# Kernel tuning notes

Measured on AMD Instinct MI355X. Metric: run time of the kernel, lower is better.

Reference implementation:

```python
import jax, jax.numpy as jnp
import numpy as np

IMAGE_W = 256
IMAGE_H = 256
SIGMA = 0.2
EPS = 1e-07


def _gauss_filter(g, size, psize, pad):
    """g: [B,N] center coords in pixels. Returns [B,N,size,psize]."""
    # grid coords over padded canvas: value i - pad at row i (matches np.indices - pad)
    coords = jnp.arange(size + 2 * pad, dtype=jnp.float32) - pad          # [size+2pad]
    offs = jnp.arange(1, psize + 1, dtype=jnp.float32) - psize / 2 - 0.5  # [psize]
    mu = g[:, :, None] + offs[None, None, :]                              # [B,N,psize]
    F = jnp.exp(-(coords[None, None, :, None] - mu[:, :, None, :]) ** 2 / (2 * SIGMA ** 2))
    F = F / (F.sum(axis=2, keepdims=True) + EPS)
    return F[:, :, pad:size + pad]                                        # [B,N,size,psize]


def setup_inputs() -> dict:
    key = jax.random.key(0)
    k1, k2 = jax.random.split(key)
    brushes = jax.random.uniform(k1, (32, 64, 2), dtype=jnp.float32)
    patches = jax.random.normal(k2, (32, 64, 3, 16, 16), dtype=jnp.float32)
    return {"brushes": brushes, "patches": patches}


def reference(brushes, patches):
    B, N, C, ph, pw = patches.shape
    pad = ph // 2  # pad='half_patch'
    gx = brushes[:, :, 0] * IMAGE_W  # [B,N]
    gy = brushes[:, :, 1] * IMAGE_H
    Fx = _gauss_filter(gx, IMAGE_W, pw, pad)  # [B,N,w,pw]
    Fy = _gauss_filter(gy, IMAGE_H, ph, pad)  # [B,N,h,ph]
    # contract over pw: [B,N,C,w,ph]
    t = jnp.einsum('bnwq,bncpq->bncwp', Fx, patches)
    # contract over ph: [B,N,C,w,h]
    out = jnp.einsum('bncwp,bnhp->bncwh', t, Fy)
    out = out.mean(axis=1)            # [B,C,w,h]
    out = jnp.swapaxes(out, 2, 3)     # [B,C,h,w]
    return out
```

## Files before the change

### kernel.cpp

```cpp
#include <hip/hip_runtime.h>
#include <hip/hip_bf16.h>


#define E25 1.3887944e-11f

__global__ __launch_bounds__(256) void brush_prep(
        const float* __restrict__ brushes,
        const float* __restrict__ patches,
        float* __restrict__ patchP)
{
    const int bn   = blockIdx.x;
    const int tid  = threadIdx.x;
    const int lane = tid & 63;
    const int qi   = tid & 15;
    const int pi   = tid >> 4;

    const float2 g = ((const float2*)brushes)[bn];
    const float gx = g.x * 256.0f, gy = g.y * 256.0f;

    const int k = lane & 31;
    const float gg = (k >> 4) ? gy : gx;
    const float mu = gg + (float)(k & 15) - 7.5f;
    const float fl = floorf(mu);
    float Z = 0.0f;
#pragma unroll
    for (int d = -1; d <= 2; ++d) {
        const float c = fl + (float)d;
        if (c >= -8.0f && c <= 263.0f) {
            const float u = c - mu;
            Z += __expf(-12.5f * u * u);
        }
    }
    const float invz = 1.0f / (Z + 1e-7f);
    const float s = __shfl(invz, qi, 64) * __shfl(invz, 16 + pi, 64);

    const float* pb = patches + (size_t)bn * 768;
    float*       wp = patchP  + (size_t)bn * 768;
    wp[tid]       = pb[tid]       * s;
    wp[tid + 256] = pb[tid + 256] * s;
    wp[tid + 512] = pb[tid + 512] * s;
}

__global__ __launch_bounds__(256) void brush_tile(
        const float* __restrict__ brushes,
        const float* __restrict__ patchP,
        float* __restrict__ out)
{
    const int b    = blockIdx.z;
    const int tx   = blockIdx.x << 4;
    const int ty   = blockIdx.y << 4;
    const int tid  = threadIdx.x;
    const int lane = tid & 63;
    const int qi   = tid & 15;
    const int pi   = tid >> 4;
    const int w    = tx + qi;
    const int h    = ty + pi;

    __shared__ float4 T4[2 * 16 * 21];

    if (tid < 160) {
        const int buf = tid / 80, r = tid % 80;
        T4[buf * 336 + (r / 5) * 21 + 16 + (r % 5)] = make_float4(0, 0, 0, 0);
    }

    const float2 g0 = ((const float2*)brushes)[(b << 6) + lane];
    const float bx = g0.x * 256.0f, by = g0.y * 256.0f;
    const bool hit =
        (bx >= (float)tx - 9.5f) & (bx <= (float)tx + 24.5f) &
        (by >= (float)ty - 9.5f) & (by <= (float)ty + 24.5f);
    unsigned long long mask = __ballot(hit);

    float acc0 = 0.0f, acc1 = 0.0f, acc2 = 0.0f;

    if (mask) {
        int n = __builtin_ctzll(mask);
        mask &= mask - 1;
        const float* wp = patchP + (size_t)((b << 6) + n) * 768;
        float a0 = wp[tid], a1 = wp[tid + 256], a2 = wp[tid + 512];
        int it = 0;

        while (true) {
            int nn = -1;
            float p0, p1, p2;
            if (mask) {
                nn = __builtin_ctzll(mask);
                mask &= mask - 1;
                const float* wq = patchP + (size_t)((b << 6) + nn) * 768;
                p0 = wq[tid]; p1 = wq[tid + 256]; p2 = wq[tid + 512];
            }

            const float gx = __shfl(bx, n, 64);
            const float gy = __shfl(by, n, 64);
            const int buf = (it & 1) * 336;

            {
                const float ax  = (float)w - gx + 7.5f;
                const bool  okx = (ax >= -2.5f) & (ax <= 17.5f);
                int qlo = (int)ceilf(ax - 2.0f);
                qlo = qlo < 0 ? 0 : (qlo > 15 ? 15 : qlo);
                float d0 = ax - (float)qlo;
                d0 = fminf(fmaxf(d0, -3.0f), 3.0f);
                float wgt = okx ? __expf(-12.5f * d0 * d0) : 0.0f;
                float u   = __expf(25.0f * d0 - 12.5f);
                const int base = ((pi & 3) << 4) + qlo;
                float4 s = make_float4(0, 0, 0, 0);
#pragma unroll
                for (int j = 0; j < 5; ++j) {
                    const float t0 = __shfl(a0, base + j, 64);
                    const float t1 = __shfl(a1, base + j, 64);
                    const float t2 = __shfl(a2, base + j, 64);
                    const float wj = (qlo + j < 16) ? wgt : 0.0f;
                    s.x += wj * t0; s.y += wj * t1; s.z += wj * t2;
                    wgt *= u; u *= E25;
                }
                T4[buf + qi * 21 + pi] = s;
            }
            __syncthreads();

            {
                const float ay = (float)h - gy + 7.5f;
                if (ay >= -2.5f && ay <= 17.5f) {
                    int plo = (int)ceilf(ay - 2.0f);
                    plo = plo < 0 ? 0 : (plo > 15 ? 15 : plo);
                    const float d0 = ay - (float)plo;
                    float wgt = __expf(-12.5f * d0 * d0);
                    float u   = __expf(25.0f * d0 - 12.5f);
                    const float4* row = &T4[buf + qi * 21 + plo];
#pragma unroll
                    for (int j = 0; j < 5; ++j) {
                        const float4 v = row[j];
                        acc0 += wgt * v.x; acc1 += wgt * v.y; acc2 += wgt * v.z;
                        wgt *= u; u *= E25;
                    }
                }
            }

            if (nn < 0) break;
            n = nn; a0 = p0; a1 = p1; a2 = p2; ++it;
        }
    }

    const float sc = 1.0f / 64.0f;
    float* ob = out + (((size_t)(b * 3)) << 16) + (h << 8) + w;
    ob[0]       = acc0 * sc;
    ob[1 << 16] = acc1 * sc;
    ob[2 << 16] = acc2 * sc;
}

extern "C" void kernel_launch(void* const* d_in, const int* in_sizes, int n_in,
                              void* d_out, int out_size, void* d_ws, size_t ws_size,
                              hipStream_t stream) {
    const float* brushes = (const float*)d_in[0];
    const float* patches = (const float*)d_in[1];
    float* out    = (float*)d_out;
    float* patchP = (float*)d_ws;
    brush_prep<<<dim3(32 * 64), dim3(256), 0, stream>>>(brushes, patches, patchP);
    brush_tile<<<dim3(16, 16, 32), dim3(256), 0, stream>>>(brushes, patchP, out);
}
```

Before: 81.55 us.

## Fuse patch normalization into tile kernel and process 8-tile vertical strips per block

Removes the separate prep kernel that pre-scaled patches by normalizers, computing the normalization inline per brush in the tile kernel instead. Each block now handles a 16x128 strip (8 tiles), building a compacted job list of (tile, brush) pairs in shared memory and streaming through it with prefetch, flushing accumulators per tile. This removes one launch and the workspace round-trip, but cuts the grid from 8192 to 1024 blocks. It also serializes the tiles within each block and recomputes the normalizer for every job.

New measurement: 89.68 us. +10.0%, slower.

```diff
diff --git a/kernel.cpp b/kernel.cpp
--- a/kernel.cpp
+++ b/kernel.cpp
@@ -4,59 +4,23 @@
 
 #define E25 1.3887944e-11f
 
-__global__ __launch_bounds__(256) void brush_prep(
+__global__ __launch_bounds__(256) void brush_strip(
         const float* __restrict__ brushes,
         const float* __restrict__ patches,
-        float* __restrict__ patchP)
-{
-    const int bn   = blockIdx.x;
-    const int tid  = threadIdx.x;
-    const int lane = tid & 63;
-    const int qi   = tid & 15;
-    const int pi   = tid >> 4;
-
-    const float2 g = ((const float2*)brushes)[bn];
-    const float gx = g.x * 256.0f, gy = g.y * 256.0f;
-
-    const int k = lane & 31;
-    const float gg = (k >> 4) ? gy : gx;
-    const float mu = gg + (float)(k & 15) - 7.5f;
-    const float fl = floorf(mu);
-    float Z = 0.0f;
-#pragma unroll
-    for (int d = -1; d <= 2; ++d) {
-        const float c = fl + (float)d;
-        if (c >= -8.0f && c <= 263.0f) {
-            const float u = c - mu;
-            Z += __expf(-12.5f * u * u);
-        }
-    }
-    const float invz = 1.0f / (Z + 1e-7f);
-    const float s = __shfl(invz, qi, 64) * __shfl(invz, 16 + pi, 64);
-
-    const float* pb = patches + (size_t)bn * 768;
-    float*       wp = patchP  + (size_t)bn * 768;
-    wp[tid]       = pb[tid]       * s;
-    wp[tid + 256] = pb[tid + 256] * s;
-    wp[tid + 512] = pb[tid + 512] * s;
-}
-
-__global__ __launch_bounds__(256) void brush_tile(
-        const float* __restrict__ brushes,
-        const float* __restrict__ patchP,
         float* __restrict__ out)
 {
     const int b    = blockIdx.z;
     const int tx   = blockIdx.x << 4;
-    const int ty   = blockIdx.y << 4;
+    const int ty0  = blockIdx.y << 7;
     const int tid  = threadIdx.x;
     const int lane = tid & 63;
     const int qi   = tid & 15;
     const int pi   = tid >> 4;
     const int w    = tx + qi;
-    const int h    = ty + pi;
 
     __shared__ float4 T4[2 * 16 * 21];
+    __shared__ int    jobs[192];
+    __shared__ int    njobs;
 
     if (tid < 160) {
         const int buf = tid / 80, r = tid % 80;
@@ -65,86 +29,132 @@
 
     const float2 g0 = ((const float2*)brushes)[(b << 6) + lane];
     const float bx = g0.x * 256.0f, by = g0.y * 256.0f;
-    const bool hit =
-        (bx >= (float)tx - 9.5f) & (bx <= (float)tx + 24.5f) &
-        (by >= (float)ty - 9.5f) & (by <= (float)ty + 24.5f);
-    unsigned long long mask = __ballot(hit);
 
+    if (tid < 64) {
+        int base = 0;
+        const bool hx = (bx >= (float)tx - 9.5f) & (bx <= (float)tx + 24.5f);
+#pragma unroll
+        for (int t = 0; t < 8; ++t) {
+            const float tyf = (float)(ty0 + (t << 4));
+            const bool hit = hx & (by >= tyf - 9.5f) & (by <= tyf + 24.5f);
+            const unsigned long long m = __ballot(hit);
+            const int rank = __popcll(m & ((1ull << lane) - 1ull));
+            if (hit) jobs[base + rank] = (t << 6) | lane;
+            base += __popcll(m);
+        }
+        if (tid == 0) njobs = base;
+    }
+    __syncthreads();
+
+    const int cnt = njobs;
     float acc0 = 0.0f, acc1 = 0.0f, acc2 = 0.0f;
+    int cur = 0;
+    const float sc = 1.0f / 64.0f;
+    float* const obase = out + (((size_t)(b * 3)) << 16) + tx + qi;
 
-    if (mask) {
-        int n = __builtin_ctzll(mask);
-        mask &= mask - 1;
-        const float* wp = patchP + (size_t)((b << 6) + n) * 768;
-        float a0 = wp[tid], a1 = wp[tid + 256], a2 = wp[tid + 512];
-        int it = 0;
+    int job = 0;
+    float r0, r1, r2;
+    if (cnt > 0) {
+        job = jobs[0];
+        const float* wp = patches + (size_t)((b << 6) + (job & 63)) * 768;
+        r0 = wp[tid]; r1 = wp[tid + 256]; r2 = wp[tid + 512];
+    }
 
-        while (true) {
-            int nn = -1;
-            float p0, p1, p2;
-            if (mask) {
-                nn = __builtin_ctzll(mask);
-                mask &= mask - 1;
-                const float* wq = patchP + (size_t)((b << 6) + nn) * 768;
-                p0 = wq[tid]; p1 = wq[tid + 256]; p2 = wq[tid + 512];
+    for (int j = 0; j < cnt; ++j) {
+        int njob = -1; float n0, n1, n2;
+        if (j + 1 < cnt) {
+            njob = jobs[j + 1];
+            const float* wq = patches + (size_t)((b << 6) + (njob & 63)) * 768;
+            n0 = wq[tid]; n1 = wq[tid + 256]; n2 = wq[tid + 512];
+        }
+
+        const int t = job >> 6, n = job & 63;
+
+        while (cur < t) {
+            float* ob = obase + ((ty0 + (cur << 4) + pi) << 8);
+            ob[0] = acc0 * sc; ob[1 << 16] = acc1 * sc; ob[2 << 16] = acc2 * sc;
+            acc0 = acc1 = acc2 = 0.0f;
+            ++cur;
+        }
+
+        const float gx = __shfl(bx, n, 64);
+        const float gy = __shfl(by, n, 64);
+
+        float invz;
+        {
+            const int k = lane & 31;
+            const float g  = (k >> 4) ? gy : gx;
+            const float mu = g + (float)(k & 15) - 7.5f;
+            const float fl = floorf(mu);
+            float Z = 0.0f;
+#pragma unroll
+            for (int d = -1; d <= 2; ++d) {
+                const float c = fl + (float)d;
+                if (c >= -8.0f && c <= 263.0f) {
+                    const float u = c - mu;
+                    Z += __expf(-12.5f * u * u);
+                }
             }
+            invz = 1.0f / (Z + 1e-7f);
+        }
+        const float zx  = __shfl(invz, qi, 64);
+        const float zyp = __shfl(invz, 16 + pi, 64);
+        const float v0 = r0 * zx, v1 = r1 * zx, v2 = r2 * zx;
 
-            const float gx = __shfl(bx, n, 64);
-            const float gy = __shfl(by, n, 64);
-            const int buf = (it & 1) * 336;
+        const int buf = (j & 1) * 336;
 
-            {
-                const float ax  = (float)w - gx + 7.5f;
-                const bool  okx = (ax >= -2.5f) & (ax <= 17.5f);
-                int qlo = (int)ceilf(ax - 2.0f);
-                qlo = qlo < 0 ? 0 : (qlo > 15 ? 15 : qlo);
-                float d0 = ax - (float)qlo;
-                d0 = fminf(fmaxf(d0, -3.0f), 3.0f);
-                float wgt = okx ? __expf(-12.5f * d0 * d0) : 0.0f;
+        {
+            const float ax  = (float)w - gx + 7.5f;
+            const bool  okx = (ax >= -2.5f) & (ax <= 17.5f);
+            int qlo = (int)ceilf(ax - 2.0f);
+            qlo = qlo < 0 ? 0 : (qlo > 15 ? 15 : qlo);
+            float d0 = ax - (float)qlo;
+            d0 = fminf(fmaxf(d0, -3.0f), 3.0f);
+            float wgt = okx ? __expf(-12.5f * d0 * d0) : 0.0f;
+            float u   = __expf(25.0f * d0 - 12.5f);
+            const int base = ((pi & 3) << 4) + qlo;
+            float4 s = make_float4(0, 0, 0, 0);
+#pragma unroll
+            for (int jj = 0; jj < 5; ++jj) {
+                const float t0 = __shfl(v0, base + jj, 64);
+                const float t1 = __shfl(v1, base + jj, 64);
+                const float t2 = __shfl(v2, base + jj, 64);
+                const float wj = (qlo + jj < 16) ? wgt : 0.0f;
+                s.x += wj * t0; s.y += wj * t1; s.z += wj * t2;
+                wgt *= u; u *= E25;
+            }
+            s.x *= zyp; s.y *= zyp; s.z *= zyp;
+            T4[buf + qi * 21 + pi] = s;
+        }
+        __syncthreads();
+
+        {
+            const float ay = (float)(ty0 + (t << 4) + pi) - gy + 7.5f;
+            if (ay >= -2.5f && ay <= 17.5f) {
+                int plo = (int)ceilf(ay - 2.0f);
+                plo = plo < 0 ? 0 : (plo > 15 ? 15 : plo);
+                const float d0 = ay - (float)plo;
+                float wgt = __expf(-12.5f * d0 * d0);
                 float u   = __expf(25.0f * d0 - 12.5f);
-                const int base = ((pi & 3) << 4) + qlo;
-                float4 s = make_float4(0, 0, 0, 0);
+                const float4* row = &T4[buf + qi * 21 + plo];
 #pragma unroll
-                for (int j = 0; j < 5; ++j) {
-                    const float t0 = __shfl(a0, base + j, 64);
-                    const float t1 = __shfl(a1, base + j, 64);
-                    const float t2 = __shfl(a2, base + j, 64);
-                    const float wj = (qlo + j < 16) ? wgt : 0.0f;
-                    s.x += wj * t0; s.y += wj * t1; s.z += wj * t2;
+                for (int jj = 0; jj < 5; ++jj) {
+                    const float4 v = row[jj];
+                    acc0 += wgt * v.x; acc1 += wgt * v.y; acc2 += wgt * v.z;
                     wgt *= u; u *= E25;
                 }
-                T4[buf + qi * 21 + pi] = s;
             }
-            __syncthreads();
+        }
 
-            {
-                const float ay = (float)h - gy + 7.5f;
-                if (ay >= -2.5f && ay <= 17.5f) {
-                    int plo = (int)ceilf(ay - 2.0f);
-                    plo = plo < 0 ? 0 : (plo > 15 ? 15 : plo);
-                    const float d0 = ay - (float)plo;
-                    float wgt = __expf(-12.5f * d0 * d0);
-                    float u   = __expf(25.0f * d0 - 12.5f);
-                    const float4* row = &T4[buf + qi * 21 + plo];
-#pragma unroll
-                    for (int j = 0; j < 5; ++j) {
-                        const float4 v = row[j];
-                        acc0 += wgt * v.x; acc1 += wgt * v.y; acc2 += wgt * v.z;
-                        wgt *= u; u *= E25;
-                    }
-                }
-            }
-
-            if (nn < 0) break;
-            n = nn; a0 = p0; a1 = p1; a2 = p2; ++it;
-        }
+        job = njob; r0 = n0; r1 = n1; r2 = n2;
     }
 
-    const float sc = 1.0f / 64.0f;
-    float* ob = out + (((size_t)(b * 3)) << 16) + (h << 8) + w;
-    ob[0]       = acc0 * sc;
-    ob[1 << 16] = acc1 * sc;
-    ob[2 << 16] = acc2 * sc;
+    while (cur < 8) {
+        float* ob = obase + ((ty0 + (cur << 4) + pi) << 8);
+        ob[0] = acc0 * sc; ob[1 << 16] = acc1 * sc; ob[2 << 16] = acc2 * sc;
+        acc0 = acc1 = acc2 = 0.0f;
+        ++cur;
+    }
 }
 
 extern "C" void kernel_launch(void* const* d_in, const int* in_sizes, int n_in,
@@ -152,8 +162,6 @@
                               hipStream_t stream) {
     const float* brushes = (const float*)d_in[0];
     const float* patches = (const float*)d_in[1];
-    float* out    = (float*)d_out;
-    float* patchP = (float*)d_ws;
-    brush_prep<<<dim3(32 * 64), dim3(256), 0, stream>>>(brushes, patches, patchP);
-    brush_tile<<<dim3(16, 16, 32), dim3(256), 0, stream>>>(brushes, patchP, out);
+    float* out = (float*)d_out;
+    brush_strip<<<dim3(16, 2, 32), dim3(256), 0, stream>>>(brushes, patches, out);
 }
```
